# Kernel tuning notes

Hardware: AMD Instinct MI355X
Metric: run time of the kernel (lower is better)

The kernel has to match this reference:

```python
import jax, jax.numpy as jnp
import numpy as np
import math

B, T, C, H = 4, 1024, 1024, 16
D = C // H  # head dim = 64

def setup_inputs() -> dict:
    key = jax.random.key(0)
    ks = jax.random.split(key, 10)
    s = 1.0 / math.sqrt(C)
    x = jax.random.normal(ks[0], (B, T, C), dtype=jnp.float32)
    pad = (jax.random.uniform(ks[1], (B, T)) < 0.2).astype(jnp.float32)
    # ensure first token of every row is unpadded so softmax rows are well-posed
    pad = pad.at[:, 0].set(0.0)
    Wq = jax.random.normal(ks[2], (C, C), dtype=jnp.float32) * s
    bq = jnp.zeros((C,), dtype=jnp.float32)
    Wk = jax.random.normal(ks[3], (C, C), dtype=jnp.float32) * s
    bk = jnp.zeros((C,), dtype=jnp.float32)
    Wv = jax.random.normal(ks[4], (C, C), dtype=jnp.float32) * s
    bv = jnp.zeros((C,), dtype=jnp.float32)
    Wp = jax.random.normal(ks[5], (C, C), dtype=jnp.float32) * s
    bp = jnp.zeros((C,), dtype=jnp.float32)
    return {"x": x, "x_padding_judge": pad, "Wq": Wq, "bq": bq,
            "Wk": Wk, "bk": bk, "Wv": Wv, "bv": bv, "Wp": Wp, "bp": bp}

def reference(x, x_padding_judge, Wq, bq, Wk, bk, Wv, bv, Wp, bp):
    # keep flag: 1.0 where token is real, 0.0 where padded
    keep = 1.0 - x_padding_judge                      # [B, T]
    mask = keep[:, :, None] * keep[:, None, :]        # [B, T, T] outer product
    # projections, split heads: [B, H, T, D]
    def heads(w, b):
        return (x @ w + b).reshape(B, T, H, D).transpose(0, 2, 1, 3)
    q, k, v = heads(Wq, bq), heads(Wk, bk), heads(Wv, bv)
    att = jnp.einsum('bhqd,bhkd->bhqk', q, k) * (1.0 / math.sqrt(D))
    # attn_pdrop=0 => att_full is all ones; masked_fill where mask == 0
    att = jnp.where(mask[:, None, :, :] == 0, -1e9, att)
    att = jax.nn.softmax(att, axis=-1)
    y = jnp.einsum('bhqk,bhkd->bhqd', att, v)         # [B, H, T, D]
    y = y.transpose(0, 2, 1, 3).reshape(B, T, C)
    return y @ Wp + bp
```

## Files before the change

kernel.cpp:

```cpp
#include <hip/hip_runtime.h>
#include <hip/hip_bf16.h>
#include <math.h>

#define Bb 4
#define Tt 1024
#define Cc 1024
#define Hh 16
#define Dd 64

typedef __attribute__((ext_vector_type(8))) _Float16 half8;
typedef __attribute__((ext_vector_type(4))) _Float16 half4;
typedef __attribute__((ext_vector_type(4))) float floatx4;


__device__ __forceinline__ void gl2lds16(const void* g, void* l) {
    __builtin_amdgcn_global_load_lds(
        (const __attribute__((address_space(1))) void*)g,
        (__attribute__((address_space(3))) void*)l,
        16, 0, 0);
}

__global__ __launch_bounds__(256) void convert_fp16(const float* __restrict__ s,
                                                    _Float16* __restrict__ d)
{
    const int m16 = blockIdx.x;
    const int r   = threadIdx.x & 15;
    const int kc0 = threadIdx.x >> 4;
    const float* src = s + (size_t)(m16 * 16 + r) * 1024;
    _Float16*   dst = d + (size_t)m16 * 16384 + r * 8;
#pragma unroll
    for (int c8 = 0; c8 < 8; ++c8) {
        const int kc = kc0 + c8 * 16;
        float4 a = *(const float4*)(src + kc * 8);
        float4 b = *(const float4*)(src + kc * 8 + 4);
        half8 h;
        h[0] = (_Float16)a.x; h[1] = (_Float16)a.y; h[2] = (_Float16)a.z; h[3] = (_Float16)a.w;
        h[4] = (_Float16)b.x; h[5] = (_Float16)b.y; h[6] = (_Float16)b.z; h[7] = (_Float16)b.w;
        *(half8*)(dst + kc * 128) = h;
    }
}

struct WPrep { const float* W[4]; _Float16* out[4]; };

__global__ __launch_bounds__(256) void prep_weights(WPrep p)
{
    const int z = blockIdx.z;
    const float* __restrict__ W = p.W[z];
    _Float16* __restrict__ outp = p.out[z];
    __shared__ float tile[64][65];
    const int k0  = blockIdx.y * 64;
    const int n0  = blockIdx.x * 64;
    const int tr  = threadIdx.x >> 4;
    const int tc4 = (threadIdx.x & 15) * 4;

#pragma unroll
    for (int i = 0; i < 4; ++i) {
        const int kk = tr + i * 16;
        float4 v = *(const float4*)(W + (size_t)(k0 + kk) * 1024 + n0 + tc4);
        tile[kk][tc4 + 0] = v.x;
        tile[kk][tc4 + 1] = v.y;
        tile[kk][tc4 + 2] = v.z;
        tile[kk][tc4 + 3] = v.w;
    }
    __syncthreads();
#pragma unroll
    for (int i = 0; i < 4; ++i) {
        half4 h;
#pragma unroll
        for (int c = 0; c < 4; ++c) h[c] = (_Float16)tile[tc4 + c][tr + i * 16];
        _Float16* dst = outp + (size_t)((n0 >> 4) + i) * 16384
                        + ((k0 + tc4) >> 3) * 128 + tr * 8 + (tc4 & 7);
        *(half4*)dst = h;
    }
}

struct QkvP { const _Float16* Wt[3]; const float* bias[3];
              _Float16* qb; _Float16* kb; _Float16* vt; };

__global__ __launch_bounds__(256) void gemm_qkv(const _Float16* __restrict__ xh, QkvP p)
{
    const int z = blockIdx.z;
    const _Float16* __restrict__ Wt   = p.Wt[z];
    const float* __restrict__    bias = p.bias[z];

    const int tid  = threadIdx.x;
    const int lane = tid & 63;
    const int w    = tid >> 6;
    const int wr   = w >> 1, wc = w & 1;
    const int quad = lane >> 4;
    const int l15  = lane & 15;
    const int bm   = blockIdx.x * 128;
    const int bn   = blockIdx.y * 128;

    const _Float16* Ap[4];
    const _Float16* Bp[4];
#pragma unroll
    for (int i = 0; i < 4; ++i)
        Ap[i] = xh + (size_t)((bm >> 4) + wr * 4 + i) * 16384 + lane * 8;
#pragma unroll
    for (int j = 0; j < 4; ++j)
        Bp[j] = Wt + (size_t)((bn >> 4) + wc * 4 + j) * 16384 + lane * 8;

    floatx4 acc[4][4];
#pragma unroll
    for (int i = 0; i < 4; ++i)
#pragma unroll
        for (int j = 0; j < 4; ++j)
            acc[i][j] = (floatx4){0.f, 0.f, 0.f, 0.f};

    half8 a0[4], b0[4];
#pragma unroll
    for (int i = 0; i < 4; ++i) a0[i] = *(const half8*)(Ap[i]);
#pragma unroll
    for (int j = 0; j < 4; ++j) b0[j] = *(const half8*)(Bp[j]);

    for (int kt = 0; kt < 1024; kt += 64) {
        half8 a1[4], b1[4];
        const size_t o1 = (size_t)(kt + 32) * 16;
#pragma unroll
        for (int i = 0; i < 4; ++i) a1[i] = *(const half8*)(Ap[i] + o1);
#pragma unroll
        for (int j = 0; j < 4; ++j) b1[j] = *(const half8*)(Bp[j] + o1);
#pragma unroll
        for (int i = 0; i < 4; ++i)
#pragma unroll
            for (int j = 0; j < 4; ++j)
                acc[i][j] = __builtin_amdgcn_mfma_f32_16x16x32_f16(a0[i], b0[j], acc[i][j], 0, 0, 0);

        const size_t o2 = (kt + 64 < 1024) ? (size_t)(kt + 64) * 16 : 0;
#pragma unroll
        for (int i = 0; i < 4; ++i) a0[i] = *(const half8*)(Ap[i] + o2);
#pragma unroll
        for (int j = 0; j < 4; ++j) b0[j] = *(const half8*)(Bp[j] + o2);
#pragma unroll
        for (int i = 0; i < 4; ++i)
#pragma unroll
            for (int j = 0; j < 4; ++j)
                acc[i][j] = __builtin_amdgcn_mfma_f32_16x16x32_f16(a1[i], b1[j], acc[i][j], 0, 0, 0);
    }

    if (z == 2) {
#pragma unroll
        for (int j = 0; j < 4; ++j) {
            const int col = bn + wc * 64 + j * 16 + l15;
            const int h = col >> 6, dd = col & 63;
            const float bj = bias[col];
#pragma unroll
            for (int i = 0; i < 4; ++i) {
                const int t0 = bm + wr * 64 + i * 16 + quad * 4;
                const int bi = t0 >> 10, t = t0 & 1023;
                half4 pk;
#pragma unroll
                for (int r = 0; r < 4; ++r) pk[r] = (_Float16)(acc[i][j][r] + bj);
                *(half4*)(p.vt + ((size_t)(bi * 16 + h) * 64 + dd) * 1024 + t) = pk;
            }
        }
    } else {
        _Float16* outp = (z == 0) ? p.qb : p.kb;
#pragma unroll
        for (int j = 0; j < 4; ++j) {
            const int col = bn + wc * 64 + j * 16 + l15;
            const int h = col >> 6, dd = col & 63;
            const float bj = bias[col];
#pragma unroll
            for (int i = 0; i < 4; ++i) {
#pragma unroll
                for (int r = 0; r < 4; ++r) {
                    const int tg = bm + wr * 64 + i * 16 + quad * 4 + r;
                    const int bi = tg >> 10, t = tg & 1023;
                    outp[((size_t)(bi * 16 + h) * 1024 + t) * 64 + dd] =
                        (_Float16)(acc[i][j][r] + bj);
                }
            }
        }
    }
}

__global__ __launch_bounds__(256) void attn_mfma(
    const _Float16* __restrict__ qb, const _Float16* __restrict__ kb,
    const _Float16* __restrict__ vt, const float* __restrict__ padj,
    _Float16* __restrict__ yh)
{
    __shared__ __align__(16) _Float16 Qs[8192];
    __shared__ __align__(16) _Float16 Ks[4096];
    __shared__ __align__(16) _Float16 Vt[4096];
    __shared__ __align__(16) _Float16 Ps[8192];
    __shared__ float keepq_s[128];
    __shared__ float keepk_s[64];

    const int tid  = threadIdx.x;
    const int lane = tid & 63;
    const int w    = tid >> 6;
    const int quad = lane >> 4;
    const int l15  = lane & 15;
    const int bh   = blockIdx.x;
    const int q0   = blockIdx.y * 128;
    const int b    = bh >> 4;
    const int h    = bh & 15;

    const _Float16* qbase = qb + (size_t)bh * Tt * Dd;
    const _Float16* kbase = kb + (size_t)bh * Tt * Dd;
    const _Float16* vbase = vt + (size_t)bh * Dd * Tt;

#pragma unroll
    for (int it = 0; it < 4; ++it) {
        const int c = it * 256 + tid;
        const int row = c & 127, kc = c >> 7;
        gl2lds16(qbase + (size_t)(q0 + row) * 64 + kc * 8, Qs + (c >> 6) * 512);
    }
    if (tid < 128) keepq_s[tid] = 1.0f - padj[b * Tt + q0 + tid];

    floatx4 O[2][4];
    floatx4 l_acc[2];
#pragma unroll
    for (int mi = 0; mi < 2; ++mi) {
#pragma unroll
        for (int dj = 0; dj < 4; ++dj) O[mi][dj] = (floatx4){0.f, 0.f, 0.f, 0.f};
        l_acc[mi] = (floatx4){0.f, 0.f, 0.f, 0.f};
    }

    half8 ones;
#pragma unroll
    for (int j = 0; j < 8; ++j) ones[j] = (_Float16)1.0f;

    constexpr float SC = 0.18033688011112042f;

    for (int kt = 0; kt < Tt; kt += 64) {
        __syncthreads();

#pragma unroll
        for (int it = 0; it < 2; ++it) {
            const int c = it * 256 + tid;
            const int key = c & 63, kc = c >> 6;
            gl2lds16(kbase + (size_t)(kt + key) * 64 + kc * 8, Ks + (c >> 6) * 512);
        }
#pragma unroll
        for (int it = 0; it < 2; ++it) {
            const int c = it * 256 + tid;
            const int dd = c & 63, kc = c >> 6;
            gl2lds16(vbase + (size_t)dd * 1024 + kt + kc * 8, Vt + (c >> 6) * 512);
        }
        if (tid < 64) keepk_s[tid] = 1.0f - padj[b * Tt + kt + tid];
        __syncthreads();

        floatx4 ST[4][2];
#pragma unroll
        for (int mk = 0; mk < 4; ++mk)
#pragma unroll
            for (int nq = 0; nq < 2; ++nq)
                ST[mk][nq] = (floatx4){0.f, 0.f, 0.f, 0.f};
#pragma unroll
        for (int ks = 0; ks < 2; ++ks) {
            half8 ak[4], bq[2];
#pragma unroll
            for (int mk = 0; mk < 4; ++mk)
                ak[mk] = *(const half8*)&Ks[((ks * 4 + quad) * 64 + mk * 16 + l15) * 8];
#pragma unroll
            for (int nq = 0; nq < 2; ++nq)
                bq[nq] = *(const half8*)&Qs[((ks * 4 + quad) * 128 + w * 32 + nq * 16 + l15) * 8];
#pragma unroll
            for (int mk = 0; mk < 4; ++mk)
#pragma unroll
                for (int nq = 0; nq < 2; ++nq)
                    ST[mk][nq] = __builtin_amdgcn_mfma_f32_16x16x32_f16(ak[mk], bq[nq], ST[mk][nq], 0, 0, 0);
        }

        const float kq0 = keepq_s[w * 32 + l15];
        const float kq1 = keepq_s[w * 32 + 16 + l15];
#pragma unroll
        for (int mk = 0; mk < 4; ++mk) {
            const float4 kk4 = *(const float4*)&keepk_s[mk * 16 + quad * 4];
            const float kkr[4] = {kk4.x, kk4.y, kk4.z, kk4.w};
#pragma unroll
            for (int nq = 0; nq < 2; ++nq) {
                const float kq = nq ? kq1 : kq0;
                half4 pk;
#pragma unroll
                for (int r = 0; r < 4; ++r) {
                    const float e = __builtin_amdgcn_exp2f(ST[mk][nq][r] * SC);
                    const float p = (kq == 0.0f) ? 1.0f : kkr[r] * e;
                    pk[r] = (_Float16)p;
                }
                *(half4*)&Ps[((mk * 2 + (quad >> 1)) * 128 + w * 32 + nq * 16 + l15) * 8 + (quad & 1) * 4] = pk;
            }
        }
        __syncthreads();

#pragma unroll
        for (int ks = 0; ks < 2; ++ks) {
            half8 ap[2], bv[4];
#pragma unroll
            for (int mi = 0; mi < 2; ++mi)
                ap[mi] = *(const half8*)&Ps[((ks * 4 + quad) * 128 + w * 32 + mi * 16 + l15) * 8];
#pragma unroll
            for (int dj = 0; dj < 4; ++dj)
                bv[dj] = *(const half8*)&Vt[((ks * 4 + quad) * 64 + dj * 16 + l15) * 8];
#pragma unroll
            for (int mi = 0; mi < 2; ++mi) {
#pragma unroll
                for (int dj = 0; dj < 4; ++dj)
                    O[mi][dj] = __builtin_amdgcn_mfma_f32_16x16x32_f16(ap[mi], bv[dj], O[mi][dj], 0, 0, 0);
                l_acc[mi] = __builtin_amdgcn_mfma_f32_16x16x32_f16(ap[mi], ones, l_acc[mi], 0, 0, 0);
            }
        }
    }

#pragma unroll
    for (int mi = 0; mi < 2; ++mi) {
#pragma unroll
        for (int r = 0; r < 4; ++r) {
            const int rowl  = w * 32 + mi * 16 + quad * 4 + r;
            const int token = b * Tt + q0 + rowl;
            const float inv = 1.0f / l_acc[mi][r];
            const size_t tb = (size_t)(token >> 4) * 16384 + (token & 15) * 8;
#pragma unroll
            for (int dj = 0; dj < 4; ++dj) {
                const int col = h * 64 + dj * 16 + l15;
                yh[tb + (col >> 3) * 128 + (col & 7)] = (_Float16)(O[mi][dj][r] * inv);
            }
        }
    }
}

__global__ __launch_bounds__(256) void gemm_proj(const _Float16* __restrict__ Ay,
                                                 const _Float16* __restrict__ Bt,
                                                 const float* __restrict__ bias,
                                                 float* __restrict__ out)
{
    const int tid  = threadIdx.x;
    const int lane = tid & 63;
    const int w    = tid >> 6;
    const int quad = lane >> 4;
    const int l15  = lane & 15;
    const int bm   = blockIdx.x * 128;
    const int bn   = blockIdx.y * 64;

    const _Float16* Ap[2];
    const _Float16* Bp[4];
#pragma unroll
    for (int i = 0; i < 2; ++i)
        Ap[i] = Ay + (size_t)((bm >> 4) + w * 2 + i) * 16384 + lane * 8;
#pragma unroll
    for (int j = 0; j < 4; ++j)
        Bp[j] = Bt + (size_t)((bn >> 4) + j) * 16384 + lane * 8;

    floatx4 acc[2][4];
#pragma unroll
    for (int i = 0; i < 2; ++i)
#pragma unroll
        for (int j = 0; j < 4; ++j)
            acc[i][j] = (floatx4){0.f, 0.f, 0.f, 0.f};

    half8 a0[2], b0[4];
#pragma unroll
    for (int i = 0; i < 2; ++i) a0[i] = *(const half8*)(Ap[i]);
#pragma unroll
    for (int j = 0; j < 4; ++j) b0[j] = *(const half8*)(Bp[j]);

    for (int kt = 0; kt < 1024; kt += 64) {
        half8 a1[2], b1[4];
        const size_t o1 = (size_t)(kt + 32) * 16;
#pragma unroll
        for (int i = 0; i < 2; ++i) a1[i] = *(const half8*)(Ap[i] + o1);
#pragma unroll
        for (int j = 0; j < 4; ++j) b1[j] = *(const half8*)(Bp[j] + o1);
#pragma unroll
        for (int i = 0; i < 2; ++i)
#pragma unroll
            for (int j = 0; j < 4; ++j)
                acc[i][j] = __builtin_amdgcn_mfma_f32_16x16x32_f16(a0[i], b0[j], acc[i][j], 0, 0, 0);

        const size_t o2 = (kt + 64 < 1024) ? (size_t)(kt + 64) * 16 : 0;
#pragma unroll
        for (int i = 0; i < 2; ++i) a0[i] = *(const half8*)(Ap[i] + o2);
#pragma unroll
        for (int j = 0; j < 4; ++j) b0[j] = *(const half8*)(Bp[j] + o2);
#pragma unroll
        for (int i = 0; i < 2; ++i)
#pragma unroll
            for (int j = 0; j < 4; ++j)
                acc[i][j] = __builtin_amdgcn_mfma_f32_16x16x32_f16(a1[i], b1[j], acc[i][j], 0, 0, 0);
    }

#pragma unroll
    for (int j = 0; j < 4; ++j) {
        const int col = bn + j * 16 + l15;
        const float bj = bias[col];
#pragma unroll
        for (int i = 0; i < 2; ++i) {
            const int row = bm + w * 32 + i * 16 + quad * 4;
            float* o = out + (size_t)row * 1024 + col;
#pragma unroll
            for (int r = 0; r < 4; ++r)
                o[(size_t)r * 1024] = acc[i][j][r] + bj;
        }
    }
}

extern "C" void kernel_launch(void* const* d_in, const int* in_sizes, int n_in,
                              void* d_out, int out_size, void* d_ws, size_t ws_size,
                              hipStream_t stream)
{
    const float* x    = (const float*)d_in[0];
    const float* padj = (const float*)d_in[1];
    const float* Wq   = (const float*)d_in[2];
    const float* bq   = (const float*)d_in[3];
    const float* Wk   = (const float*)d_in[4];
    const float* bk   = (const float*)d_in[5];
    const float* Wv   = (const float*)d_in[6];
    const float* bv   = (const float*)d_in[7];
    const float* Wp   = (const float*)d_in[8];
    const float* bp   = (const float*)d_in[9];
    float* out = (float*)d_out;

    const size_t MB = 1024 * 1024;
    char* ws = (char*)d_ws;
    _Float16* xh  = (_Float16*)(ws);
    _Float16* Wt0 = (_Float16*)(ws +  8 * MB);
    _Float16* Wt1 = (_Float16*)(ws + 10 * MB);
    _Float16* Wt2 = (_Float16*)(ws + 12 * MB);
    _Float16* Wtp = (_Float16*)(ws + 14 * MB);
    _Float16* qb  = (_Float16*)(ws + 16 * MB);
    _Float16* kb  = (_Float16*)(ws + 24 * MB);
    _Float16* vtb = (_Float16*)(ws + 32 * MB);
    _Float16* yh  = (_Float16*)(ws + 40 * MB);

    convert_fp16<<<256, 256, 0, stream>>>(x, xh);

    WPrep wp;
    wp.W[0] = Wq; wp.W[1] = Wk; wp.W[2] = Wv; wp.W[3] = Wp;
    wp.out[0] = Wt0; wp.out[1] = Wt1; wp.out[2] = Wt2; wp.out[3] = Wtp;
    prep_weights<<<dim3(16, 16, 4), 256, 0, stream>>>(wp);

    QkvP qp;
    qp.Wt[0] = Wt0; qp.Wt[1] = Wt1; qp.Wt[2] = Wt2;
    qp.bias[0] = bq; qp.bias[1] = bk; qp.bias[2] = bv;
    qp.qb = qb; qp.kb = kb; qp.vt = vtb;
    gemm_qkv<<<dim3(32, 8, 3), 256, 0, stream>>>(xh, qp);

    attn_mfma<<<dim3(64, 8), 256, 0, stream>>>(qb, kb, vtb, padj, yh);

    gemm_proj<<<dim3(32, 16), 256, 0, stream>>>(yh, Wtp, bp, out);
}
```

Baseline: 189.0 us.

## Store Q/K/V in MFMA-fragment layout and load attention operands directly from global

The QKV projection epilogue now writes Q, K and the transposed V in a pre-swizzled layout that matches the MFMA fragment ordering. This lets the attention kernel load its operands with contiguous per-lane 16-byte global loads straight into registers. Shared-memory staging of Q/K/V and the block-wide barriers are removed, and each wave keeps only a private P buffer in LDS. The aim is to cut LDS traffic and synchronisation. The cost is that each wave re-reads K/V from global/L2 with no sharing across waves, and the scattered epilogue stores become less coalesced.

```diff
diff --git a/kernel.cpp b/kernel.cpp
--- a/kernel.cpp
+++ b/kernel.cpp
@@ -12,13 +12,6 @@
 typedef __attribute__((ext_vector_type(4))) _Float16 half4;
 typedef __attribute__((ext_vector_type(4))) float floatx4;
 
-
-__device__ __forceinline__ void gl2lds16(const void* g, void* l) {
-    __builtin_amdgcn_global_load_lds(
-        (const __attribute__((address_space(1))) void*)g,
-        (__attribute__((address_space(3))) void*)l,
-        16, 0, 0);
-}
 
 __global__ __launch_bounds__(256) void convert_fp16(const float* __restrict__ s,
                                                     _Float16* __restrict__ d)
@@ -143,16 +136,18 @@
 #pragma unroll
         for (int j = 0; j < 4; ++j) {
             const int col = bn + wc * 64 + j * 16 + l15;
-            const int h = col >> 6, dd = col & 63;
+            const int h  = col >> 6;
             const float bj = bias[col];
 #pragma unroll
             for (int i = 0; i < 4; ++i) {
                 const int t0 = bm + wr * 64 + i * 16 + quad * 4;
-                const int bi = t0 >> 10, t = t0 & 1023;
+                const int bh = (t0 >> 10) * 16 + h;
+                const int tm = t0 & 1023;
                 half4 pk;
 #pragma unroll
                 for (int r = 0; r < 4; ++r) pk[r] = (_Float16)(acc[i][j][r] + bj);
-                *(half4*)(p.vt + ((size_t)(bi * 16 + h) * 64 + dd) * 1024 + t) = pk;
+                *(half4*)(p.vt + (size_t)bh * 65536 + (size_t)j * 16384
+                          + (tm >> 3) * 128 + l15 * 8 + (tm & 7)) = pk;
             }
         }
     } else {
@@ -160,15 +155,18 @@
 #pragma unroll
         for (int j = 0; j < 4; ++j) {
             const int col = bn + wc * 64 + j * 16 + l15;
-            const int h = col >> 6, dd = col & 63;
+            const int h  = col >> 6;
+            const int dd = col & 63;
             const float bj = bias[col];
+            const int doff = (dd >> 3) * 128 + (dd & 7);
 #pragma unroll
             for (int i = 0; i < 4; ++i) {
 #pragma unroll
                 for (int r = 0; r < 4; ++r) {
                     const int tg = bm + wr * 64 + i * 16 + quad * 4 + r;
-                    const int bi = tg >> 10, t = tg & 1023;
-                    outp[((size_t)(bi * 16 + h) * 1024 + t) * 64 + dd] =
+                    const int bh = (tg >> 10) * 16 + h;
+                    const int tm = tg & 1023;
+                    outp[(size_t)bh * 65536 + (tm >> 4) * 1024 + doff + (tm & 15) * 8] =
                         (_Float16)(acc[i][j][r] + bj);
                 }
             }
@@ -181,12 +179,7 @@
     const _Float16* __restrict__ vt, const float* __restrict__ padj,
     _Float16* __restrict__ yh)
 {
-    __shared__ __align__(16) _Float16 Qs[8192];
-    __shared__ __align__(16) _Float16 Ks[4096];
-    __shared__ __align__(16) _Float16 Vt[4096];
-    __shared__ __align__(16) _Float16 Ps[8192];
-    __shared__ float keepq_s[128];
-    __shared__ float keepk_s[64];
+    __shared__ __align__(16) _Float16 Ps[4][2048];
 
     const int tid  = threadIdx.x;
     const int lane = tid & 63;
@@ -198,17 +191,22 @@
     const int b    = bh >> 4;
     const int h    = bh & 15;
 
-    const _Float16* qbase = qb + (size_t)bh * Tt * Dd;
-    const _Float16* kbase = kb + (size_t)bh * Tt * Dd;
-    const _Float16* vbase = vt + (size_t)bh * Dd * Tt;
-
-#pragma unroll
-    for (int it = 0; it < 4; ++it) {
-        const int c = it * 256 + tid;
-        const int row = c & 127, kc = c >> 7;
-        gl2lds16(qbase + (size_t)(q0 + row) * 64 + kc * 8, Qs + (c >> 6) * 512);
-    }
-    if (tid < 128) keepq_s[tid] = 1.0f - padj[b * Tt + q0 + tid];
+    const _Float16* qf = qb + (size_t)bh * 65536;
+    const _Float16* kf = kb + (size_t)bh * 65536;
+    const _Float16* vf = vt + (size_t)bh * 65536;
+    const float*    pk_row = padj + b * Tt;
+
+    half8 bq[2][2];
+#pragma unroll
+    for (int ks = 0; ks < 2; ++ks)
+#pragma unroll
+        for (int nq = 0; nq < 2; ++nq)
+            bq[ks][nq] = *(const half8*)(qf + (size_t)((q0 >> 4) + w * 2 + nq) * 1024
+                                         + ks * 512 + lane * 8);
+    float kq[2];
+#pragma unroll
+    for (int nq = 0; nq < 2; ++nq)
+        kq[nq] = 1.0f - pk_row[q0 + w * 32 + nq * 16 + l15];
 
     floatx4 O[2][4];
     floatx4 l_acc[2];
@@ -218,7 +216,6 @@
         for (int dj = 0; dj < 4; ++dj) O[mi][dj] = (floatx4){0.f, 0.f, 0.f, 0.f};
         l_acc[mi] = (floatx4){0.f, 0.f, 0.f, 0.f};
     }
-
     half8 ones;
 #pragma unroll
     for (int j = 0; j < 8; ++j) ones[j] = (_Float16)1.0f;
@@ -226,22 +223,23 @@
     constexpr float SC = 0.18033688011112042f;
 
     for (int kt = 0; kt < Tt; kt += 64) {
-        __syncthreads();
-
-#pragma unroll
-        for (int it = 0; it < 2; ++it) {
-            const int c = it * 256 + tid;
-            const int key = c & 63, kc = c >> 6;
-            gl2lds16(kbase + (size_t)(kt + key) * 64 + kc * 8, Ks + (c >> 6) * 512);
-        }
-#pragma unroll
-        for (int it = 0; it < 2; ++it) {
-            const int c = it * 256 + tid;
-            const int dd = c & 63, kc = c >> 6;
-            gl2lds16(vbase + (size_t)dd * 1024 + kt + kc * 8, Vt + (c >> 6) * 512);
-        }
-        if (tid < 64) keepk_s[tid] = 1.0f - padj[b * Tt + kt + tid];
-        __syncthreads();
+        half8 ak[2][4], bv[2][4];
+#pragma unroll
+        for (int ks = 0; ks < 2; ++ks)
+#pragma unroll
+            for (int mk = 0; mk < 4; ++mk)
+                ak[ks][mk] = *(const half8*)(kf + (size_t)((kt >> 4) + mk) * 1024
+                                             + ks * 512 + lane * 8);
+#pragma unroll
+        for (int ks = 0; ks < 2; ++ks)
+#pragma unroll
+            for (int dj = 0; dj < 4; ++dj)
+                bv[ks][dj] = *(const half8*)(vf + (size_t)dj * 16384 + (kt >> 3) * 128
+                                             + ks * 512 + lane * 8);
+        float4 kk4[4];
+#pragma unroll
+        for (int mk = 0; mk < 4; ++mk)
+            kk4[mk] = *(const float4*)(pk_row + kt + mk * 16 + quad * 4);
 
         floatx4 ST[4][2];
 #pragma unroll
@@ -250,57 +248,46 @@
             for (int nq = 0; nq < 2; ++nq)
                 ST[mk][nq] = (floatx4){0.f, 0.f, 0.f, 0.f};
 #pragma unroll
-        for (int ks = 0; ks < 2; ++ks) {
-            half8 ak[4], bq[2];
+        for (int ks = 0; ks < 2; ++ks)
 #pragma unroll
             for (int mk = 0; mk < 4; ++mk)
-                ak[mk] = *(const half8*)&Ks[((ks * 4 + quad) * 64 + mk * 16 + l15) * 8];
-#pragma unroll
-            for (int nq = 0; nq < 2; ++nq)
-                bq[nq] = *(const half8*)&Qs[((ks * 4 + quad) * 128 + w * 32 + nq * 16 + l15) * 8];
-#pragma unroll
-            for (int mk = 0; mk < 4; ++mk)
 #pragma unroll
                 for (int nq = 0; nq < 2; ++nq)
-                    ST[mk][nq] = __builtin_amdgcn_mfma_f32_16x16x32_f16(ak[mk], bq[nq], ST[mk][nq], 0, 0, 0);
-        }
-
-        const float kq0 = keepq_s[w * 32 + l15];
-        const float kq1 = keepq_s[w * 32 + 16 + l15];
+                    ST[mk][nq] = __builtin_amdgcn_mfma_f32_16x16x32_f16(
+                        ak[ks][mk], bq[ks][nq], ST[mk][nq], 0, 0, 0);
+
 #pragma unroll
         for (int mk = 0; mk < 4; ++mk) {
-            const float4 kk4 = *(const float4*)&keepk_s[mk * 16 + quad * 4];
-            const float kkr[4] = {kk4.x, kk4.y, kk4.z, kk4.w};
+            const float kkr[4] = {1.0f - kk4[mk].x, 1.0f - kk4[mk].y,
+                                  1.0f - kk4[mk].z, 1.0f - kk4[mk].w};
 #pragma unroll
             for (int nq = 0; nq < 2; ++nq) {
-                const float kq = nq ? kq1 : kq0;
                 half4 pk;
 #pragma unroll
                 for (int r = 0; r < 4; ++r) {
                     const float e = __builtin_amdgcn_exp2f(ST[mk][nq][r] * SC);
-                    const float p = (kq == 0.0f) ? 1.0f : kkr[r] * e;
-                    pk[r] = (_Float16)p;
+                    const float pv = (kq[nq] == 0.0f) ? 1.0f : kkr[r] * e;
+                    pk[r] = (_Float16)pv;
                 }
-                *(half4*)&Ps[((mk * 2 + (quad >> 1)) * 128 + w * 32 + nq * 16 + l15) * 8 + (quad & 1) * 4] = pk;
+                *(half4*)&Ps[w][((mk * 2 + (quad >> 1)) * 32 + nq * 16 + l15) * 8
+                               + (quad & 1) * 4] = pk;
             }
         }
-        __syncthreads();
 
 #pragma unroll
         for (int ks = 0; ks < 2; ++ks) {
-            half8 ap[2], bv[4];
+            half8 ap[2];
 #pragma unroll
             for (int mi = 0; mi < 2; ++mi)
-                ap[mi] = *(const half8*)&Ps[((ks * 4 + quad) * 128 + w * 32 + mi * 16 + l15) * 8];
-#pragma unroll
-            for (int dj = 0; dj < 4; ++dj)
-                bv[dj] = *(const half8*)&Vt[((ks * 4 + quad) * 64 + dj * 16 + l15) * 8];
+                ap[mi] = *(const half8*)&Ps[w][((ks * 4 + quad) * 32 + mi * 16 + l15) * 8];
 #pragma unroll
             for (int mi = 0; mi < 2; ++mi) {
 #pragma unroll
                 for (int dj = 0; dj < 4; ++dj)
-                    O[mi][dj] = __builtin_amdgcn_mfma_f32_16x16x32_f16(ap[mi], bv[dj], O[mi][dj], 0, 0, 0);
-                l_acc[mi] = __builtin_amdgcn_mfma_f32_16x16x32_f16(ap[mi], ones, l_acc[mi], 0, 0, 0);
+                    O[mi][dj] = __builtin_amdgcn_mfma_f32_16x16x32_f16(
+                        ap[mi], bv[ks][dj], O[mi][dj], 0, 0, 0);
+                l_acc[mi] = __builtin_amdgcn_mfma_f32_16x16x32_f16(
+                    ap[mi], ones, l_acc[mi], 0, 0, 0);
             }
         }
     }
```

New measurement: 188.6 us. No clear change (-0.2%).
